# Optimization experiments

Hardware: AMD Instinct MI355X
Metric: run time of the kernel (lower is better)

## Reference

```python
import jax, jax.numpy as jnp
import numpy as np

N = 50000
E = 800000
H = 4
C = 64
EPS = 1e-5

def _gat_layer(x, W, a_src, a_dst, bias, src, dst, n):
    # x: [N, F_in]; W: [F_in, H*C]
    h = (x @ W).reshape(n, H, C)                      # [N,H,C]
    asrc = jnp.einsum('nhc,hc->nh', h, a_src)         # [N,H]
    adst = jnp.einsum('nhc,hc->nh', h, a_dst)         # [N,H]
    e = jax.nn.leaky_relu(asrc[src] + adst[dst], 0.2) # [E,H]
    emax = jax.ops.segment_max(e, dst, num_segments=n)
    e = jnp.exp(e - emax[dst])
    denom = jax.ops.segment_sum(e, dst, num_segments=n)
    alpha = e / (denom[dst] + 1e-16)                  # [E,H]
    msg = h[src] * alpha[:, :, None]                  # [E,H,C]
    out = jax.ops.segment_sum(msg, dst, num_segments=n)
    return out.reshape(n, H * C) + bias

def _bn_eval(x, gamma, beta, mean, var):
    return (x - mean) * jax.lax.rsqrt(var + EPS) * gamma + beta

def setup_inputs() -> dict:
    key = jax.random.key(0)
    ks = jax.random.split(key, 12)
    d = {}
    d['x'] = jax.random.normal(ks[0], (N, 128), jnp.float32)
    d['edge_index'] = jax.random.randint(ks[1], (2, E), 0, N, jnp.int32)
    d['W1'] = jax.random.normal(ks[2], (128, H * C), jnp.float32) * 0.05
    d['a_src1'] = jax.random.normal(ks[3], (H, C), jnp.float32) * 0.05
    d['a_dst1'] = jax.random.normal(ks[4], (H, C), jnp.float32) * 0.05
    d['b1'] = jnp.zeros((H * C,), jnp.float32)
    d['g1'] = jax.random.uniform(ks[5], (H * C,), jnp.float32, 0.5, 1.5)
    d['be1'] = jnp.zeros((H * C,), jnp.float32)
    d['m1'] = jnp.zeros((H * C,), jnp.float32)
    d['v1'] = jax.random.uniform(ks[6], (H * C,), jnp.float32, 0.5, 1.5)
    d['W2'] = jax.random.normal(ks[7], (H * C, H * C), jnp.float32) * 0.05
    d['a_src2'] = jax.random.normal(ks[8], (H, C), jnp.float32) * 0.05
    d['a_dst2'] = jax.random.normal(ks[9], (H, C), jnp.float32) * 0.05
    d['b2'] = jnp.zeros((H * C,), jnp.float32)
    d['g2'] = jax.random.uniform(ks[10], (H * C,), jnp.float32, 0.5, 1.5)
    d['be2'] = jnp.zeros((H * C,), jnp.float32)
    d['m2'] = jnp.zeros((H * C,), jnp.float32)
    d['v2'] = jax.random.uniform(ks[11], (H * C,), jnp.float32, 0.5, 1.5)
    return d

def reference(x, edge_index, W1, a_src1, a_dst1, b1, g1, be1, m1, v1,
              W2, a_src2, a_dst2, b2, g2, be2, m2, v2):
    # PyG GATConv default: add self-loops
    loops = jnp.arange(N, dtype=edge_index.dtype)
    src = jnp.concatenate([edge_index[0], loops])
    dst = jnp.concatenate([edge_index[1], loops])
    h = _gat_layer(x, W1, a_src1, a_dst1, b1, src, dst, N)
    h = jax.nn.relu(_bn_eval(h, g1, be1, m1, v1))  # dropout identity at eval
    h = _gat_layer(h, W2, a_src2, a_dst2, b2, src, dst, N)
    h = jax.nn.relu(_bn_eval(h, g2, be2, m2, v2))
    return jax.nn.log_softmax(h, axis=1)
```

## Files before the change

### kernel.cpp

```cpp
#include <hip/hip_runtime.h>
#include <hip/hip_bf16.h>
#include <cstdint>

#define N_NODES 50000
#define N_EDGES 800000
#define ET_EDGES (N_EDGES + N_NODES)
#define FDIM 256
#define BN_EPS 1e-5f
#define CAP 96

typedef short bf16x8 __attribute__((ext_vector_type(8)));
typedef float f32x4 __attribute__((ext_vector_type(4)));

__device__ __forceinline__ float lrelu(float x) { return x >= 0.f ? x : 0.2f * x; }
__device__ __forceinline__ unsigned short f2b(float f) {
    unsigned int u = __float_as_uint(f);
    u += 0x7fffu + ((u >> 16) & 1u);
    return (unsigned short)(u >> 16);
}

__device__ __forceinline__ void acc_u8(float acc8[8], int2 p, float c) {
    unsigned px = (unsigned)p.x, py = (unsigned)p.y;
#pragma unroll
    for (int k = 0; k < 4; ++k)
        acc8[k] = fmaf((float)((unsigned char)(px >> (8 * k))), c, acc8[k]);
#pragma unroll
    for (int k = 0; k < 4; ++k)
        acc8[k + 4] = fmaf((float)((unsigned char)(py >> (8 * k))), c, acc8[k + 4]);
}

#define PB_Z  196
#define PB_W1 128
#define PB_W2 256
__global__ __launch_bounds__(256) void prep_kernel(
        const float* __restrict__ W1, unsigned short* __restrict__ W1T,
        const float* __restrict__ W2, unsigned short* __restrict__ W2T,
        int* __restrict__ cursor,
        const float* __restrict__ b1, const float* __restrict__ g1,
        const float* __restrict__ be1, const float* __restrict__ m1,
        const float* __restrict__ v1,
        const float* __restrict__ b2, const float* __restrict__ g2,
        const float* __restrict__ be2, const float* __restrict__ m2,
        const float* __restrict__ v2,
        float* sc1, float* sh1, float* sc2, float* sh2) {
    int b = blockIdx.x, tid = threadIdx.x;
    if (b < PB_Z) {
        int i = b * 256 + tid;
        if (i < N_NODES) cursor[i] = 0;
    } else if (b < PB_Z + PB_W1) {
        int t = (b - PB_Z) * 256 + tid;
        int n = t >> 7, k = t & 127;
        W1T[t] = f2b(W1[(size_t)k * 256 + n]);
    } else if (b < PB_Z + PB_W1 + PB_W2) {
        int t = (b - PB_Z - PB_W1) * 256 + tid;
        int n = t >> 8, k = t & 255;
        W2T[t] = f2b(W2[(size_t)k * 256 + n]);
    } else {
        int f = tid;
        float s1 = rsqrtf(v1[f] + BN_EPS) * g1[f];
        sc1[f] = s1;
        sh1[f] = (b1[f] - m1[f]) * s1 + be1[f];
        float s2 = rsqrtf(v2[f] + BN_EPS) * g2[f];
        sc2[f] = s2;
        sh2[f] = (b2[f] - m2[f]) * s2 + be2[f];
    }
}

#define SG_GEMM 782
#define SG_SCAT 3321
#define SG_MIX  (2 * SG_GEMM)
__global__ __launch_bounds__(256) void scat_gemm1_kernel(
        const int* __restrict__ ei, int* __restrict__ cursor, int* __restrict__ csr,
        const float* __restrict__ x,
        const unsigned short* __restrict__ BT,
        const float* __restrict__ a_src, const float* __restrict__ a_dst,
        signed char* __restrict__ H8, float* __restrict__ scaleRow,
        float* __restrict__ asrc, float* __restrict__ adst, int M) {
    constexpr int K = 128;
    constexpr int BK = 64;
    __shared__ unsigned short As[64][BK + 8];
    __shared__ unsigned short Bs[256][BK + 8];
    __shared__ int amaxL[64];
    const int tid = threadIdx.x;
    const int b = blockIdx.x;

    int gemmIdx = -1, scatIdx = 0;
    if (b < SG_MIX) { if (b & 1) gemmIdx = b >> 1; else scatIdx = b >> 1; }
    else scatIdx = b - SG_GEMM;

    if (gemmIdx < 0) {
        int e = scatIdx * 256 + tid;
        if (e < ET_EDGES) {
            int s, d;
            if (e < N_EDGES) { s = ei[e]; d = ei[N_EDGES + e]; }
            else             { s = d = e - N_EDGES; }
            int pos = atomicAdd(&cursor[d], 1);
            if (pos < CAP) csr[d * CAP + pos] = s;
        }
        return;
    }

    const int lane = tid & 63;
    const int w = tid >> 6;
    const int bm = gemmIdx * 64;
    const int wc = w * 64;
    const int hd = w;
    if (tid < 64) amaxL[tid] = 0;

    f32x4 acc[4][4];
#pragma unroll
    for (int i = 0; i < 4; ++i)
#pragma unroll
        for (int j = 0; j < 4; ++j) acc[i][j] = (f32x4){0.f, 0.f, 0.f, 0.f};

    const int srow = tid >> 3;
    const int skc = (tid & 7) * 8;

    for (int k0 = 0; k0 < K; k0 += BK) {
#pragma unroll
        for (int i = 0; i < 2; ++i) {
            int row = i * 32 + srow;
            int ar = bm + row; if (ar >= M) ar = M - 1;
            const float* xp = x + (size_t)ar * K + k0 + skc;
            float4 v0 = *(const float4*)xp;
            float4 v1 = *(const float4*)(xp + 4);
            bf16x8 o;
            o[0] = (short)f2b(v0.x); o[1] = (short)f2b(v0.y);
            o[2] = (short)f2b(v0.z); o[3] = (short)f2b(v0.w);
            o[4] = (short)f2b(v1.x); o[5] = (short)f2b(v1.y);
            o[6] = (short)f2b(v1.z); o[7] = (short)f2b(v1.w);
            *(bf16x8*)&As[row][skc] = o;
        }
#pragma unroll
        for (int i = 0; i < 8; ++i) {
            int row = i * 32 + srow;
            *(bf16x8*)&Bs[row][skc] = *(const bf16x8*)(BT + (size_t)row * K + k0 + skc);
        }
        __syncthreads();
#pragma unroll
        for (int ks = 0; ks < BK; ks += 32) {
            const int kk = ks + (lane >> 4) * 8;
            bf16x8 af[4], bfr[4];
#pragma unroll
            for (int i = 0; i < 4; ++i) {
                af[i]  = *(const bf16x8*)&As[i * 16 + (lane & 15)][kk];
                bfr[i] = *(const bf16x8*)&Bs[wc + i * 16 + (lane & 15)][kk];
            }
#pragma unroll
            for (int i = 0; i < 4; ++i)
#pragma unroll
                for (int j = 0; j < 4; ++j)
                    acc[i][j] = __builtin_amdgcn_mfma_f32_16x16x32_bf16(af[i], bfr[j], acc[i][j], 0, 0, 0);
        }
        __syncthreads();
    }

    const int q = lane >> 4, c16 = lane & 15;
#pragma unroll
    for (int i = 0; i < 4; ++i) {
#pragma unroll
        for (int r = 0; r < 4; ++r) {
            float a = fmaxf(fmaxf(fabsf(acc[i][0][r]), fabsf(acc[i][1][r])),
                            fmaxf(fabsf(acc[i][2][r]), fabsf(acc[i][3][r])));
#pragma unroll
            for (int off = 1; off < 16; off <<= 1) a = fmaxf(a, __shfl_xor(a, off));
            if (c16 == 0) atomicMax(&amaxL[i * 16 + q * 4 + r], __float_as_int(a));
        }
    }
    __syncthreads();

    float asv[4], adv[4];
#pragma unroll
    for (int j = 0; j < 4; ++j) {
        int c = j * 16 + c16;
        asv[j] = a_src[hd * 64 + c];
        adv[j] = a_dst[hd * 64 + c];
    }
#pragma unroll
    for (int i = 0; i < 4; ++i) {
#pragma unroll
        for (int r = 0; r < 4; ++r) {
            int lrow = i * 16 + q * 4 + r;
            int gr = bm + lrow;
            float amax = __int_as_float(amaxL[lrow]);
            float rcpS = amax > 1e-20f ? 127.f / amax : 0.f;
            if (gr < M) {
#pragma unroll
                for (int j = 0; j < 4; ++j) {
                    int qv = (int)rintf(acc[i][j][r] * rcpS);
                    H8[(size_t)gr * 256 + wc + j * 16 + c16] =
                        (signed char)(unsigned char)(qv + 128);
                }
                if (c16 == 0 && w == 0) scaleRow[gr] = amax * (1.f / 127.f);
            }
            float p_s = acc[i][0][r] * asv[0] + acc[i][1][r] * asv[1]
                      + acc[i][2][r] * asv[2] + acc[i][3][r] * asv[3];
            float p_d = acc[i][0][r] * adv[0] + acc[i][1][r] * adv[1]
                      + acc[i][2][r] * adv[2] + acc[i][3][r] * adv[3];
#pragma unroll
            for (int off = 1; off < 16; off <<= 1) {
                p_s += __shfl_xor(p_s, off);
                p_d += __shfl_xor(p_d, off);
            }
            if (c16 == 0 && gr < M) {
                asrc[(size_t)gr * 4 + hd] = p_s;
                adst[(size_t)gr * 4 + hd] = p_d;
            }
        }
    }
}

template <int K>
__global__ __launch_bounds__(256) void gemm_fused_kernel(
        const unsigned short* __restrict__ A,
        const unsigned short* __restrict__ BT,
        const float* __restrict__ a_src, const float* __restrict__ a_dst,
        signed char* __restrict__ H8, float* __restrict__ scaleRow,
        float* __restrict__ asrc, float* __restrict__ adst, int M) {
    constexpr int BK = 64;
    __shared__ unsigned short As[64][BK + 8];
    __shared__ unsigned short Bs[256][BK + 8];
    __shared__ int amaxL[64];
    const int tid = threadIdx.x;
    const int lane = tid & 63;
    const int w = tid >> 6;
    const int bm = blockIdx.x * 64;
    const int wc = w * 64;
    const int hd = w;
    if (tid < 64) amaxL[tid] = 0;

    f32x4 acc[4][4];
#pragma unroll
    for (int i = 0; i < 4; ++i)
#pragma unroll
        for (int j = 0; j < 4; ++j) acc[i][j] = (f32x4){0.f, 0.f, 0.f, 0.f};

    const int srow = tid >> 3;
    const int skc = (tid & 7) * 8;

    for (int k0 = 0; k0 < K; k0 += BK) {
#pragma unroll
        for (int i = 0; i < 2; ++i) {
            int row = i * 32 + srow;
            int ar = bm + row; if (ar >= M) ar = M - 1;
            *(bf16x8*)&As[row][skc] = *(const bf16x8*)(A + (size_t)ar * K + k0 + skc);
        }
#pragma unroll
        for (int i = 0; i < 8; ++i) {
            int row = i * 32 + srow;
            *(bf16x8*)&Bs[row][skc] = *(const bf16x8*)(BT + (size_t)row * K + k0 + skc);
        }
        __syncthreads();
#pragma unroll
        for (int ks = 0; ks < BK; ks += 32) {
            const int kk = ks + (lane >> 4) * 8;
            bf16x8 af[4], bfr[4];
#pragma unroll
            for (int i = 0; i < 4; ++i) {
                af[i]  = *(const bf16x8*)&As[i * 16 + (lane & 15)][kk];
                bfr[i] = *(const bf16x8*)&Bs[wc + i * 16 + (lane & 15)][kk];
            }
#pragma unroll
            for (int i = 0; i < 4; ++i)
#pragma unroll
                for (int j = 0; j < 4; ++j)
                    acc[i][j] = __builtin_amdgcn_mfma_f32_16x16x32_bf16(af[i], bfr[j], acc[i][j], 0, 0, 0);
        }
        __syncthreads();
    }

    const int q = lane >> 4, c16 = lane & 15;
#pragma unroll
    for (int i = 0; i < 4; ++i) {
#pragma unroll
        for (int r = 0; r < 4; ++r) {
            float a = fmaxf(fmaxf(fabsf(acc[i][0][r]), fabsf(acc[i][1][r])),
                            fmaxf(fabsf(acc[i][2][r]), fabsf(acc[i][3][r])));
#pragma unroll
            for (int off = 1; off < 16; off <<= 1) a = fmaxf(a, __shfl_xor(a, off));
            if (c16 == 0) atomicMax(&amaxL[i * 16 + q * 4 + r], __float_as_int(a));
        }
    }
    __syncthreads();

    float asv[4], adv[4];
#pragma unroll
    for (int j = 0; j < 4; ++j) {
        int c = j * 16 + c16;
        asv[j] = a_src[hd * 64 + c];
        adv[j] = a_dst[hd * 64 + c];
    }
#pragma unroll
    for (int i = 0; i < 4; ++i) {
#pragma unroll
        for (int r = 0; r < 4; ++r) {
            int lrow = i * 16 + q * 4 + r;
            int gr = bm + lrow;
            float amax = __int_as_float(amaxL[lrow]);
            float rcpS = amax > 1e-20f ? 127.f / amax : 0.f;
            if (gr < M) {
#pragma unroll
                for (int j = 0; j < 4; ++j) {
                    int qv = (int)rintf(acc[i][j][r] * rcpS);
                    H8[(size_t)gr * 256 + wc + j * 16 + c16] =
                        (signed char)(unsigned char)(qv + 128);
                }
                if (c16 == 0 && w == 0) scaleRow[gr] = amax * (1.f / 127.f);
            }
            float p_s = acc[i][0][r] * asv[0] + acc[i][1][r] * asv[1]
                      + acc[i][2][r] * asv[2] + acc[i][3][r] * asv[3];
            float p_d = acc[i][0][r] * adv[0] + acc[i][1][r] * adv[1]
                      + acc[i][2][r] * adv[2] + acc[i][3][r] * adv[3];
#pragma unroll
            for (int off = 1; off < 16; off <<= 1) {
                p_s += __shfl_xor(p_s, off);
                p_d += __shfl_xor(p_d, off);
            }
            if (c16 == 0 && gr < M) {
                asrc[(size_t)gr * 4 + hd] = p_s;
                adst[(size_t)gr * 4 + hd] = p_d;
            }
        }
    }
}

template <bool FINAL>
__device__ __forceinline__ void gat_epilogue(const float acc8[8], int fl, bool doStore,
                                             int node, const float* __restrict__ scale,
                                             const float* __restrict__ shift,
                                             float* __restrict__ outf,
                                             unsigned short* __restrict__ outb) {
    float4 scA = ((const float4*)scale)[fl * 2], scB = ((const float4*)scale)[fl * 2 + 1];
    float4 shA = ((const float4*)shift)[fl * 2], shB = ((const float4*)shift)[fl * 2 + 1];
    float t[8];
    t[0] = fmaxf(fmaf(acc8[0], scA.x, shA.x), 0.f);
    t[1] = fmaxf(fmaf(acc8[1], scA.y, shA.y), 0.f);
    t[2] = fmaxf(fmaf(acc8[2], scA.z, shA.z), 0.f);
    t[3] = fmaxf(fmaf(acc8[3], scA.w, shA.w), 0.f);
    t[4] = fmaxf(fmaf(acc8[4], scB.x, shB.x), 0.f);
    t[5] = fmaxf(fmaf(acc8[5], scB.y, shB.y), 0.f);
    t[6] = fmaxf(fmaf(acc8[6], scB.z, shB.z), 0.f);
    t[7] = fmaxf(fmaf(acc8[7], scB.w, shB.w), 0.f);
    if (FINAL) {
        float m = t[0];
#pragma unroll
        for (int k = 1; k < 8; ++k) m = fmaxf(m, t[k]);
#pragma unroll
        for (int off = 1; off < 32; off <<= 1) m = fmaxf(m, __shfl_xor(m, off));
        float es = 0.f;
#pragma unroll
        for (int k = 0; k < 8; ++k) es += __expf(t[k] - m);
#pragma unroll
        for (int off = 1; off < 32; off <<= 1) es += __shfl_xor(es, off);
        float lse = m + logf(es);
        if (doStore) {
            float* p = outf + (size_t)node * 256 + fl * 8;
            *(float4*)p = make_float4(t[0] - lse, t[1] - lse, t[2] - lse, t[3] - lse);
            *(float4*)(p + 4) = make_float4(t[4] - lse, t[5] - lse, t[6] - lse, t[7] - lse);
        }
    } else {
        if (doStore) {
            bf16x8 ob;
#pragma unroll
            for (int k = 0; k < 8; ++k) ob[k] = (short)f2b(t[k]);
            *(bf16x8*)(outb + (size_t)node * 256 + fl * 8) = ob;
        }
    }
}

template <bool FINAL>
__global__ __launch_bounds__(256) void gat_gather_kernel(
        const int* __restrict__ cursor,
        const int* __restrict__ csr,
        const float* __restrict__ asrc,
        const float* __restrict__ adst,
        const float* __restrict__ scaleRow,
        const signed char* __restrict__ h8,
        const float* __restrict__ scale,
        const float* __restrict__ shift,
        float* __restrict__ outf,
        unsigned short* __restrict__ outb) {
    __shared__ int2 sa[4][4][65];

    const int wid = threadIdx.x >> 6;
    const int lane = threadIdx.x & 63;
    const int g = lane >> 5, l32 = lane & 31;
    const int hsel = l32 >> 3;
    const unsigned fo = (unsigned)(l32 << 3);

    const int nodeBase = blockIdx.x * 8 + wid * 2;
    if (nodeBase >= N_NODES) return;

    {
        int node = nodeBase + g;
        bool valid = node < N_NODES;
        int nodeC = valid ? node : N_NODES - 1;
        int deg = valid ? min(cursor[nodeC], CAP) : 0;
        int beg = nodeC * CAP;
        int dmax = max(deg, __shfl_xor(deg, 32));

        if (dmax <= 32) {
            float4 ad = *(const float4*)(adst + (size_t)nodeC * 4);
            int s = 0;
            float sc = 0.f;
            float c0 = -3.4e38f, c1 = -3.4e38f, c2 = -3.4e38f, c3 = -3.4e38f;
            if (l32 < deg) {
                s = csr[beg + l32];
                sc = scaleRow[s];
                float4 as = *(const float4*)(asrc + (size_t)s * 4);
                c0 = lrelu(as.x + ad.x); c1 = lrelu(as.y + ad.y);
                c2 = lrelu(as.z + ad.z); c3 = lrelu(as.w + ad.w);
            }
            float m0 = c0, m1 = c1, m2 = c2, m3 = c3;
#pragma unroll
            for (int off = 1; off < 32; off <<= 1) {
                m0 = fmaxf(m0, __shfl_xor(m0, off)); m1 = fmaxf(m1, __shfl_xor(m1, off));
                m2 = fmaxf(m2, __shfl_xor(m2, off)); m3 = fmaxf(m3, __shfl_xor(m3, off));
            }
            float e0 = 0.f, e1 = 0.f, e2 = 0.f, e3 = 0.f;
            if (l32 < deg) {
                e0 = __expf(c0 - m0); e1 = __expf(c1 - m1);
                e2 = __expf(c2 - m2); e3 = __expf(c3 - m3);
            }
            float s0 = e0, s1 = e1, s2 = e2, s3 = e3;
#pragma unroll
            for (int off = 1; off < 32; off <<= 1) {
                s0 += __shfl_xor(s0, off); s1 += __shfl_xor(s1, off);
                s2 += __shfl_xor(s2, off); s3 += __shfl_xor(s3, off);
            }
            float a0 = e0 / (s0 + 1e-16f) * sc, a1 = e1 / (s1 + 1e-16f) * sc;
            float a2 = e2 / (s2 + 1e-16f) * sc, a3 = e3 / (s3 + 1e-16f) * sc;
            sa[wid][0][lane] = make_int2(s, __float_as_int(a0));
            sa[wid][1][lane] = make_int2(s, __float_as_int(a1));
            sa[wid][2][lane] = make_int2(s, __float_as_int(a2));
            sa[wid][3][lane] = make_int2(s, __float_as_int(a3));
            float t0 = a0, t1 = a1, t2 = a2, t3 = a3;
#pragma unroll
            for (int off = 1; off < 32; off <<= 1) {
                t0 += __shfl_xor(t0, off); t1 += __shfl_xor(t1, off);
                t2 += __shfl_xor(t2, off); t3 += __shfl_xor(t3, off);
            }
            float corr = 128.f * (hsel == 0 ? t0 : hsel == 1 ? t1 : hsel == 2 ? t2 : t3);
            __asm__ volatile("s_waitcnt lgkmcnt(0)" ::: "memory");

            const int2* sal = &sa[wid][hsel][g * 32];
            float acc8[8];
#pragma unroll
            for (int k = 0; k < 8; ++k) acc8[k] = 0.f;

            int e = 0;
            for (; e + 7 < deg; e += 8) {
                int2 sv[8]; int2 hv[8];
#pragma unroll
                for (int u = 0; u < 8; ++u) sv[u] = sal[e + u];
#pragma unroll
                for (int u = 0; u < 8; ++u)
                    hv[u] = *(const int2*)(h8 + (((unsigned)sv[u].x << 8) + fo));
#pragma unroll
                for (int u = 0; u < 8; ++u) acc_u8(acc8, hv[u], __int_as_float(sv[u].y));
            }
            for (; e + 3 < deg; e += 4) {
                int2 sv[4]; int2 hv[4];
#pragma unroll
                for (int u = 0; u < 4; ++u) sv[u] = sal[e + u];
#pragma unroll
                for (int u = 0; u < 4; ++u)
                    hv[u] = *(const int2*)(h8 + (((unsigned)sv[u].x << 8) + fo));
#pragma unroll
                for (int u = 0; u < 4; ++u) acc_u8(acc8, hv[u], __int_as_float(sv[u].y));
            }
            for (; e < deg; ++e) {
                int2 sv = sal[e];
                int2 hA = *(const int2*)(h8 + (((unsigned)sv.x << 8) + fo));
                acc_u8(acc8, hA, __int_as_float(sv.y));
            }
#pragma unroll
            for (int k = 0; k < 8; ++k) acc8[k] -= corr;
            gat_epilogue<FINAL>(acc8, l32, valid, node, scale, shift, outf, outb);
            return;
        }
    }

    for (int t = 0; t < 2; ++t) {
        int fnode = nodeBase + t;
        if (fnode >= N_NODES) break;
        int fdeg = min(cursor[fnode], CAP);
        int fbeg = fnode * CAP, fend = fbeg + fdeg;
        float4 ad = *(const float4*)(adst + (size_t)fnode * 4);
        float acc8[8];
#pragma unroll
        for (int k = 0; k < 8; ++k) acc8[k] = 0.f;
        float corr;

        if (fdeg <= 64) {
            int s = 0;
            float sc = 0.f;
            float c0 = -3.4e38f, c1 = -3.4e38f, c2 = -3.4e38f, c3 = -3.4e38f;
            if (lane < fdeg) {
                s = csr[fbeg + lane];
                sc = scaleRow[s];
                float4 as = *(const float4*)(asrc + (size_t)s * 4);
                c0 = lrelu(as.x + ad.x); c1 = lrelu(as.y + ad.y);
                c2 = lrelu(as.z + ad.z); c3 = lrelu(as.w + ad.w);
            }
            float m0 = c0, m1 = c1, m2 = c2, m3 = c3;
#pragma unroll
            for (int off = 1; off < 64; off <<= 1) {
                m0 = fmaxf(m0, __shfl_xor(m0, off)); m1 = fmaxf(m1, __shfl_xor(m1, off));
                m2 = fmaxf(m2, __shfl_xor(m2, off)); m3 = fmaxf(m3, __shfl_xor(m3, off));
            }
            float e0 = 0.f, e1 = 0.f, e2 = 0.f, e3 = 0.f;
            if (lane < fdeg) {
                e0 = __expf(c0 - m0); e1 = __expf(c1 - m1);
                e2 = __expf(c2 - m2); e3 = __expf(c3 - m3);
            }
            float s0 = e0, s1 = e1, s2 = e2, s3 = e3;
#pragma unroll
            for (int off = 1; off < 64; off <<= 1) {
                s0 += __shfl_xor(s0, off); s1 += __shfl_xor(s1, off);
                s2 += __shfl_xor(s2, off); s3 += __shfl_xor(s3, off);
            }
            float a0 = e0 / (s0 + 1e-16f) * sc, a1 = e1 / (s1 + 1e-16f) * sc;
            float a2 = e2 / (s2 + 1e-16f) * sc, a3 = e3 / (s3 + 1e-16f) * sc;
            sa[wid][0][lane] = make_int2(s, __float_as_int(a0));
            sa[wid][1][lane] = make_int2(s, __float_as_int(a1));
            sa[wid][2][lane] = make_int2(s, __float_as_int(a2));
            sa[wid][3][lane] = make_int2(s, __float_as_int(a3));
            float t0 = a0, t1 = a1, t2 = a2, t3 = a3;
#pragma unroll
            for (int off = 1; off < 64; off <<= 1) {
                t0 += __shfl_xor(t0, off); t1 += __shfl_xor(t1, off);
                t2 += __shfl_xor(t2, off); t3 += __shfl_xor(t3, off);
            }
            corr = 128.f * (hsel == 0 ? t0 : hsel == 1 ? t1 : hsel == 2 ? t2 : t3);
            __asm__ volatile("s_waitcnt lgkmcnt(0)" ::: "memory");

            const int2* sal = &sa[wid][hsel][0];
            int e = 0;
            for (; e + 1 < fdeg; e += 2) {
                int2 sv = sal[e + g];
                int2 hA = *(const int2*)(h8 + (((unsigned)sv.x << 8) + fo));
                acc_u8(acc8, hA, __int_as_float(sv.y));
            }
            if (e < fdeg) {
                int idx = e + g;
                int2 sv = sal[idx < fdeg ? idx : 0];
                float aA = idx < fdeg ? __int_as_float(sv.y) : 0.f;
                int2 hA = *(const int2*)(h8 + (((unsigned)sv.x << 8) + fo));
                acc_u8(acc8, hA, aA);
            }
#pragma unroll
            for (int k = 0; k < 8; ++k) acc8[k] += __shfl_xor(acc8[k], 32);
        } else {
            float m0 = -3.4e38f, m1 = -3.4e38f, m2 = -3.4e38f, m3 = -3.4e38f;
            for (int e = fbeg + lane; e < fend; e += 64) {
                int s = csr[e];
                float4 as = *(const float4*)(asrc + (size_t)s * 4);
                m0 = fmaxf(m0, lrelu(as.x + ad.x)); m1 = fmaxf(m1, lrelu(as.y + ad.y));
                m2 = fmaxf(m2, lrelu(as.z + ad.z)); m3 = fmaxf(m3, lrelu(as.w + ad.w));
            }
#pragma unroll
            for (int off = 1; off < 64; off <<= 1) {
                m0 = fmaxf(m0, __shfl_xor(m0, off)); m1 = fmaxf(m1, __shfl_xor(m1, off));
                m2 = fmaxf(m2, __shfl_xor(m2, off)); m3 = fmaxf(m3, __shfl_xor(m3, off));
            }
            float s0 = 0.f, s1 = 0.f, s2 = 0.f, s3 = 0.f;
            for (int e = fbeg + lane; e < fend; e += 64) {
                int s = csr[e];
                float4 as = *(const float4*)(asrc + (size_t)s * 4);
                s0 += __expf(lrelu(as.x + ad.x) - m0); s1 += __expf(lrelu(as.y + ad.y) - m1);
                s2 += __expf(lrelu(as.z + ad.z) - m2); s3 += __expf(lrelu(as.w + ad.w) - m3);
            }
#pragma unroll
            for (int off = 1; off < 64; off <<= 1) {
                s0 += __shfl_xor(s0, off); s1 += __shfl_xor(s1, off);
                s2 += __shfl_xor(s2, off); s3 += __shfl_xor(s3, off);
            }
            float mh = (hsel == 0) ? m0 : (hsel == 1) ? m1 : (hsel == 2) ? m2 : m3;
            float rh = (hsel == 0) ? 1.f / (s0 + 1e-16f) : (hsel == 1) ? 1.f / (s1 + 1e-16f)
                     : (hsel == 2) ? 1.f / (s2 + 1e-16f) : 1.f / (s3 + 1e-16f);
            float adh = (hsel == 0) ? ad.x : (hsel == 1) ? ad.y : (hsel == 2) ? ad.z : ad.w;
            float asumL = 0.f;
            for (int e = fbeg; e < fend; ++e) {
                int s = csr[e];
                float ash = asrc[(size_t)s * 4 + hsel];
                float a = __expf(lrelu(ash + adh) - mh) * rh * scaleRow[s];
                asumL += a;
                int2 hv = *(const int2*)(h8 + (((unsigned)s << 8) + fo));
                acc_u8(acc8, hv, a);
            }
            corr = 128.f * asumL;
        }
#pragma unroll
        for (int k = 0; k < 8; ++k) acc8[k] -= corr;
        gat_epilogue<FINAL>(acc8, l32, g == 0, fnode, scale, shift, outf, outb);
    }
}

extern "C" void kernel_launch(void* const* d_in, const int* in_sizes, int n_in,
                              void* d_out, int out_size, void* d_ws, size_t ws_size,
                              hipStream_t stream) {
    (void)in_sizes; (void)n_in; (void)out_size; (void)ws_size;
    const float* x   = (const float*)d_in[0];
    const int*   ei  = (const int*)d_in[1];
    const float* W1  = (const float*)d_in[2];
    const float* as1 = (const float*)d_in[3];
    const float* ad1 = (const float*)d_in[4];
    const float* b1  = (const float*)d_in[5];
    const float* g1  = (const float*)d_in[6];
    const float* be1 = (const float*)d_in[7];
    const float* m1  = (const float*)d_in[8];
    const float* v1  = (const float*)d_in[9];
    const float* W2  = (const float*)d_in[10];
    const float* as2 = (const float*)d_in[11];
    const float* ad2 = (const float*)d_in[12];
    const float* b2  = (const float*)d_in[13];
    const float* g2  = (const float*)d_in[14];
    const float* be2 = (const float*)d_in[15];
    const float* m2  = (const float*)d_in[16];
    const float* v2  = (const float*)d_in[17];

    float* out = (float*)d_out;
    unsigned short* actb = (unsigned short*)d_out;

    char* base = (char*)d_ws;
    signed char* h8 = (signed char*)base;          base += (size_t)N_NODES * 256;
    float* scaleRow = (float*)base;                base += (size_t)N_NODES * 4;
    base += (size_t)N_NODES * 128 * 2;
    float* asrc = (float*)base;                    base += (size_t)N_NODES * 4 * 4;
    float* adst = (float*)base;                    base += (size_t)N_NODES * 4 * 4;
    float* sc1 = (float*)base;                     base += 1024;
    float* sh1 = (float*)base;                     base += 1024;
    float* sc2 = (float*)base;                     base += 1024;
    float* sh2 = (float*)base;                     base += 1024;
    unsigned short* W1T = (unsigned short*)base;   base += 256 * 128 * 2;
    unsigned short* W2T = (unsigned short*)base;   base += 256 * 256 * 2;
    int* cursor = (int*)base;                      base += N_NODES * 4;
    int* csr  = (int*)base;

    prep_kernel<<<PB_Z + PB_W1 + PB_W2 + 1, 256, 0, stream>>>(
        W1, W1T, W2, W2T, cursor,
        b1, g1, be1, m1, v1, b2, g2, be2, m2, v2, sc1, sh1, sc2, sh2);

    const int nb = (N_NODES + 7) / 8;
    const int gb = (N_NODES + 63) / 64;

    scat_gemm1_kernel<<<SG_SCAT + SG_GEMM, 256, 0, stream>>>(
        ei, cursor, csr, x, W1T, as1, ad1, h8, scaleRow, asrc, adst, N_NODES);

    gat_gather_kernel<false><<<nb, 256, 0, stream>>>(cursor, csr, asrc, adst, scaleRow, h8,
                                                     sc1, sh1, nullptr, actb);

    gemm_fused_kernel<256><<<gb, 256, 0, stream>>>(actb, W2T, as2, ad2, h8, scaleRow,
                                                   asrc, adst, N_NODES);

    gat_gather_kernel<true><<<nb, 256, 0, stream>>>(cursor, csr, asrc, adst, scaleRow, h8,
                                                    sc2, sh2, out, nullptr);
}
```

Baseline: 291.1 us.

## Process four nodes per wave and prefetch both pairs' edge metadata up front

Each wave now handles two node pairs instead of one, halving the grid. The csr index, scaleRow, asrc and adst loads for both pairs are issued before any softmax work, so the dependent gather latency of the second pair overlaps with the first. The csr loads are now unconditional with clamped source indices, which touches padding slots. The cost is more registers, fewer waves in flight, and the second pair reusing the same LDS slot.

```diff
diff --git a/kernel.cpp b/kernel.cpp
--- a/kernel.cpp
+++ b/kernel.cpp
@@ -369,6 +369,214 @@
 }
 
 template <bool FINAL>
+__device__ __forceinline__ void gat_pair_fast(
+        int pairBase, int g, int l32, int hsel, unsigned fo,
+        bool valid, int deg, unsigned s, float sc, float4 as, float4 ad,
+        int2 (*saw)[65],
+        const signed char* __restrict__ h8,
+        const float* __restrict__ scale, const float* __restrict__ shift,
+        float* __restrict__ outf, unsigned short* __restrict__ outb) {
+    const int lane = g * 32 + l32;
+    int node = pairBase + g;
+    float c0 = -3.4e38f, c1 = -3.4e38f, c2 = -3.4e38f, c3 = -3.4e38f;
+    if (l32 < deg) {
+        c0 = lrelu(as.x + ad.x); c1 = lrelu(as.y + ad.y);
+        c2 = lrelu(as.z + ad.z); c3 = lrelu(as.w + ad.w);
+    }
+    float m0 = c0, m1 = c1, m2 = c2, m3 = c3;
+#pragma unroll
+    for (int off = 1; off < 32; off <<= 1) {
+        m0 = fmaxf(m0, __shfl_xor(m0, off)); m1 = fmaxf(m1, __shfl_xor(m1, off));
+        m2 = fmaxf(m2, __shfl_xor(m2, off)); m3 = fmaxf(m3, __shfl_xor(m3, off));
+    }
+    float e0 = 0.f, e1 = 0.f, e2 = 0.f, e3 = 0.f;
+    if (l32 < deg) {
+        e0 = __expf(c0 - m0); e1 = __expf(c1 - m1);
+        e2 = __expf(c2 - m2); e3 = __expf(c3 - m3);
+    }
+    float s0 = e0, s1 = e1, s2 = e2, s3 = e3;
+#pragma unroll
+    for (int off = 1; off < 32; off <<= 1) {
+        s0 += __shfl_xor(s0, off); s1 += __shfl_xor(s1, off);
+        s2 += __shfl_xor(s2, off); s3 += __shfl_xor(s3, off);
+    }
+    float a0 = e0 / (s0 + 1e-16f) * sc, a1 = e1 / (s1 + 1e-16f) * sc;
+    float a2 = e2 / (s2 + 1e-16f) * sc, a3 = e3 / (s3 + 1e-16f) * sc;
+    saw[0][lane] = make_int2((int)s, __float_as_int(a0));
+    saw[1][lane] = make_int2((int)s, __float_as_int(a1));
+    saw[2][lane] = make_int2((int)s, __float_as_int(a2));
+    saw[3][lane] = make_int2((int)s, __float_as_int(a3));
+    float t0 = a0, t1 = a1, t2 = a2, t3 = a3;
+#pragma unroll
+    for (int off = 1; off < 32; off <<= 1) {
+        t0 += __shfl_xor(t0, off); t1 += __shfl_xor(t1, off);
+        t2 += __shfl_xor(t2, off); t3 += __shfl_xor(t3, off);
+    }
+    float corr = 128.f * (hsel == 0 ? t0 : hsel == 1 ? t1 : hsel == 2 ? t2 : t3);
+    __asm__ volatile("s_waitcnt lgkmcnt(0)" ::: "memory");
+
+    const int2* sal = &saw[hsel][g * 32];
+    float acc8[8];
+#pragma unroll
+    for (int k = 0; k < 8; ++k) acc8[k] = 0.f;
+
+    int e = 0;
+    for (; e + 7 < deg; e += 8) {
+        int2 sv[8]; int2 hv[8];
+#pragma unroll
+        for (int u = 0; u < 8; ++u) sv[u] = sal[e + u];
+#pragma unroll
+        for (int u = 0; u < 8; ++u)
+            hv[u] = *(const int2*)(h8 + (((unsigned)sv[u].x << 8) + fo));
+#pragma unroll
+        for (int u = 0; u < 8; ++u) acc_u8(acc8, hv[u], __int_as_float(sv[u].y));
+    }
+    for (; e + 3 < deg; e += 4) {
+        int2 sv[4]; int2 hv[4];
+#pragma unroll
+        for (int u = 0; u < 4; ++u) sv[u] = sal[e + u];
+#pragma unroll
+        for (int u = 0; u < 4; ++u)
+            hv[u] = *(const int2*)(h8 + (((unsigned)sv[u].x << 8) + fo));
+#pragma unroll
+        for (int u = 0; u < 4; ++u) acc_u8(acc8, hv[u], __int_as_float(sv[u].y));
+    }
+    for (; e < deg; ++e) {
+        int2 sv = sal[e];
+        int2 hA = *(const int2*)(h8 + (((unsigned)sv.x << 8) + fo));
+        acc_u8(acc8, hA, __int_as_float(sv.y));
+    }
+#pragma unroll
+    for (int k = 0; k < 8; ++k) acc8[k] -= corr;
+    gat_epilogue<FINAL>(acc8, l32, valid, node, scale, shift, outf, outb);
+}
+
+template <bool FINAL>
+__device__ __forceinline__ void gat_pair_fallback(
+        int pairBase, int lane, int g, int l32, int hsel, unsigned fo,
+        int2 (*saw)[65],
+        const int* __restrict__ cursor, const int* __restrict__ csr,
+        const float* __restrict__ asrc, const float* __restrict__ adst,
+        const float* __restrict__ scaleRow, const signed char* __restrict__ h8,
+        const float* __restrict__ scale, const float* __restrict__ shift,
+        float* __restrict__ outf, unsigned short* __restrict__ outb) {
+    for (int t = 0; t < 2; ++t) {
+        int fnode = pairBase + t;
+        if (fnode >= N_NODES) break;
+        int fdeg = min(cursor[fnode], CAP);
+        int fbeg = fnode * CAP, fend = fbeg + fdeg;
+        float4 ad = *(const float4*)(adst + (size_t)fnode * 4);
+        float acc8[8];
+#pragma unroll
+        for (int k = 0; k < 8; ++k) acc8[k] = 0.f;
+        float corr;
+
+        if (fdeg <= 64) {
+            int s = 0;
+            float sc = 0.f;
+            float c0 = -3.4e38f, c1 = -3.4e38f, c2 = -3.4e38f, c3 = -3.4e38f;
+            if (lane < fdeg) {
+                s = csr[fbeg + lane];
+                sc = scaleRow[s];
+                float4 as = *(const float4*)(asrc + (size_t)s * 4);
+                c0 = lrelu(as.x + ad.x); c1 = lrelu(as.y + ad.y);
+                c2 = lrelu(as.z + ad.z); c3 = lrelu(as.w + ad.w);
+            }
+            float m0 = c0, m1 = c1, m2 = c2, m3 = c3;
+#pragma unroll
+            for (int off = 1; off < 64; off <<= 1) {
+                m0 = fmaxf(m0, __shfl_xor(m0, off)); m1 = fmaxf(m1, __shfl_xor(m1, off));
+                m2 = fmaxf(m2, __shfl_xor(m2, off)); m3 = fmaxf(m3, __shfl_xor(m3, off));
+            }
+            float e0 = 0.f, e1 = 0.f, e2 = 0.f, e3 = 0.f;
+            if (lane < fdeg) {
+                e0 = __expf(c0 - m0); e1 = __expf(c1 - m1);
+                e2 = __expf(c2 - m2); e3 = __expf(c3 - m3);
+            }
+            float s0 = e0, s1 = e1, s2 = e2, s3 = e3;
+#pragma unroll
+            for (int off = 1; off < 64; off <<= 1) {
+                s0 += __shfl_xor(s0, off); s1 += __shfl_xor(s1, off);
+                s2 += __shfl_xor(s2, off); s3 += __shfl_xor(s3, off);
+            }
+            float a0 = e0 / (s0 + 1e-16f) * sc, a1 = e1 / (s1 + 1e-16f) * sc;
+            float a2 = e2 / (s2 + 1e-16f) * sc, a3 = e3 / (s3 + 1e-16f) * sc;
+            saw[0][lane] = make_int2(s, __float_as_int(a0));
+            saw[1][lane] = make_int2(s, __float_as_int(a1));
+            saw[2][lane] = make_int2(s, __float_as_int(a2));
+            saw[3][lane] = make_int2(s, __float_as_int(a3));
+            float t0 = a0, t1 = a1, t2 = a2, t3 = a3;
+#pragma unroll
+            for (int off = 1; off < 64; off <<= 1) {
+                t0 += __shfl_xor(t0, off); t1 += __shfl_xor(t1, off);
+                t2 += __shfl_xor(t2, off); t3 += __shfl_xor(t3, off);
+            }
+            corr = 128.f * (hsel == 0 ? t0 : hsel == 1 ? t1 : hsel == 2 ? t2 : t3);
+            __asm__ volatile("s_waitcnt lgkmcnt(0)" ::: "memory");
+
+            const int2* sal = &saw[hsel][0];
+            int e = 0;
+            for (; e + 1 < fdeg; e += 2) {
+                int2 sv = sal[e + g];
+                int2 hA = *(const int2*)(h8 + (((unsigned)sv.x << 8) + fo));
+                acc_u8(acc8, hA, __int_as_float(sv.y));
+            }
+            if (e < fdeg) {
+                int idx = e + g;
+                int2 sv = sal[idx < fdeg ? idx : 0];
+                float aA = idx < fdeg ? __int_as_float(sv.y) : 0.f;
+                int2 hA = *(const int2*)(h8 + (((unsigned)sv.x << 8) + fo));
+                acc_u8(acc8, hA, aA);
+            }
+#pragma unroll
+            for (int k = 0; k < 8; ++k) acc8[k] += __shfl_xor(acc8[k], 32);
+        } else {
+            float m0 = -3.4e38f, m1 = -3.4e38f, m2 = -3.4e38f, m3 = -3.4e38f;
+            for (int e = fbeg + lane; e < fend; e += 64) {
+                int s = csr[e];
+                float4 as = *(const float4*)(asrc + (size_t)s * 4);
+                m0 = fmaxf(m0, lrelu(as.x + ad.x)); m1 = fmaxf(m1, lrelu(as.y + ad.y));
+                m2 = fmaxf(m2, lrelu(as.z + ad.z)); m3 = fmaxf(m3, lrelu(as.w + ad.w));
+            }
+#pragma unroll
+            for (int off = 1; off < 64; off <<= 1) {
+                m0 = fmaxf(m0, __shfl_xor(m0, off)); m1 = fmaxf(m1, __shfl_xor(m1, off));
+                m2 = fmaxf(m2, __shfl_xor(m2, off)); m3 = fmaxf(m3, __shfl_xor(m3, off));
+            }
+            float s0 = 0.f, s1 = 0.f, s2 = 0.f, s3 = 0.f;
+            for (int e = fbeg + lane; e < fend; e += 64) {
+                int s = csr[e];
+                float4 as = *(const float4*)(asrc + (size_t)s * 4);
+                s0 += __expf(lrelu(as.x + ad.x) - m0); s1 += __expf(lrelu(as.y + ad.y) - m1);
+                s2 += __expf(lrelu(as.z + ad.z) - m2); s3 += __expf(lrelu(as.w + ad.w) - m3);
+            }
+#pragma unroll
+            for (int off = 1; off < 64; off <<= 1) {
+                s0 += __shfl_xor(s0, off); s1 += __shfl_xor(s1, off);
+                s2 += __shfl_xor(s2, off); s3 += __shfl_xor(s3, off);
+            }
+            float mh = (hsel == 0) ? m0 : (hsel == 1) ? m1 : (hsel == 2) ? m2 : m3;
+            float rh = (hsel == 0) ? 1.f / (s0 + 1e-16f) : (hsel == 1) ? 1.f / (s1 + 1e-16f)
+                     : (hsel == 2) ? 1.f / (s2 + 1e-16f) : 1.f / (s3 + 1e-16f);
+            float adh = (hsel == 0) ? ad.x : (hsel == 1) ? ad.y : (hsel == 2) ? ad.z : ad.w;
+            float asumL = 0.f;
+            for (int e = fbeg; e < fend; ++e) {
+                int s = csr[e];
+                float ash = asrc[(size_t)s * 4 + hsel];
+                float a = __expf(lrelu(ash + adh) - mh) * rh * scaleRow[s];
+                asumL += a;
+                int2 hv = *(const int2*)(h8 + (((unsigned)s << 8) + fo));
+                acc_u8(acc8, hv, a);
+            }
+            corr = 128.f * asumL;
+        }
+#pragma unroll
+        for (int k = 0; k < 8; ++k) acc8[k] -= corr;
+        gat_epilogue<FINAL>(acc8, l32, g == 0, fnode, scale, shift, outf, outb);
+    }
+}
+
+template <bool FINAL>
 __global__ __launch_bounds__(256) void gat_gather_kernel(
         const int* __restrict__ cursor,
         const int* __restrict__ csr,
@@ -388,213 +596,40 @@
     const int hsel = l32 >> 3;
     const unsigned fo = (unsigned)(l32 << 3);
 
-    const int nodeBase = blockIdx.x * 8 + wid * 2;
-    if (nodeBase >= N_NODES) return;
-
-    {
-        int node = nodeBase + g;
-        bool valid = node < N_NODES;
-        int nodeC = valid ? node : N_NODES - 1;
-        int deg = valid ? min(cursor[nodeC], CAP) : 0;
-        int beg = nodeC * CAP;
-        int dmax = max(deg, __shfl_xor(deg, 32));
-
-        if (dmax <= 32) {
-            float4 ad = *(const float4*)(adst + (size_t)nodeC * 4);
-            int s = 0;
-            float sc = 0.f;
-            float c0 = -3.4e38f, c1 = -3.4e38f, c2 = -3.4e38f, c3 = -3.4e38f;
-            if (l32 < deg) {
-                s = csr[beg + l32];
-                sc = scaleRow[s];
-                float4 as = *(const float4*)(asrc + (size_t)s * 4);
-                c0 = lrelu(as.x + ad.x); c1 = lrelu(as.y + ad.y);
-                c2 = lrelu(as.z + ad.z); c3 = lrelu(as.w + ad.w);
-            }
-            float m0 = c0, m1 = c1, m2 = c2, m3 = c3;
-#pragma unroll
-            for (int off = 1; off < 32; off <<= 1) {
-                m0 = fmaxf(m0, __shfl_xor(m0, off)); m1 = fmaxf(m1, __shfl_xor(m1, off));
-                m2 = fmaxf(m2, __shfl_xor(m2, off)); m3 = fmaxf(m3, __shfl_xor(m3, off));
-            }
-            float e0 = 0.f, e1 = 0.f, e2 = 0.f, e3 = 0.f;
-            if (l32 < deg) {
-                e0 = __expf(c0 - m0); e1 = __expf(c1 - m1);
-                e2 = __expf(c2 - m2); e3 = __expf(c3 - m3);
-            }
-            float s0 = e0, s1 = e1, s2 = e2, s3 = e3;
-#pragma unroll
-            for (int off = 1; off < 32; off <<= 1) {
-                s0 += __shfl_xor(s0, off); s1 += __shfl_xor(s1, off);
-                s2 += __shfl_xor(s2, off); s3 += __shfl_xor(s3, off);
-            }
-            float a0 = e0 / (s0 + 1e-16f) * sc, a1 = e1 / (s1 + 1e-16f) * sc;
-            float a2 = e2 / (s2 + 1e-16f) * sc, a3 = e3 / (s3 + 1e-16f) * sc;
-            sa[wid][0][lane] = make_int2(s, __float_as_int(a0));
-            sa[wid][1][lane] = make_int2(s, __float_as_int(a1));
-            sa[wid][2][lane] = make_int2(s, __float_as_int(a2));
-            sa[wid][3][lane] = make_int2(s, __float_as_int(a3));
-            float t0 = a0, t1 = a1, t2 = a2, t3 = a3;
-#pragma unroll
-            for (int off = 1; off < 32; off <<= 1) {
-                t0 += __shfl_xor(t0, off); t1 += __shfl_xor(t1, off);
-                t2 += __shfl_xor(t2, off); t3 += __shfl_xor(t3, off);
-            }
-            float corr = 128.f * (hsel == 0 ? t0 : hsel == 1 ? t1 : hsel == 2 ? t2 : t3);
-            __asm__ volatile("s_waitcnt lgkmcnt(0)" ::: "memory");
-
-            const int2* sal = &sa[wid][hsel][g * 32];
-            float acc8[8];
-#pragma unroll
-            for (int k = 0; k < 8; ++k) acc8[k] = 0.f;
-
-            int e = 0;
-            for (; e + 7 < deg; e += 8) {
-                int2 sv[8]; int2 hv[8];
-#pragma unroll
-                for (int u = 0; u < 8; ++u) sv[u] = sal[e + u];
-#pragma unroll
-                for (int u = 0; u < 8; ++u)
-                    hv[u] = *(const int2*)(h8 + (((unsigned)sv[u].x << 8) + fo));
-#pragma unroll
-                for (int u = 0; u < 8; ++u) acc_u8(acc8, hv[u], __int_as_float(sv[u].y));
-            }
-            for (; e + 3 < deg; e += 4) {
-                int2 sv[4]; int2 hv[4];
-#pragma unroll
-                for (int u = 0; u < 4; ++u) sv[u] = sal[e + u];
-#pragma unroll
-                for (int u = 0; u < 4; ++u)
-                    hv[u] = *(const int2*)(h8 + (((unsigned)sv[u].x << 8) + fo));
-#pragma unroll
-                for (int u = 0; u < 4; ++u) acc_u8(acc8, hv[u], __int_as_float(sv[u].y));
-            }
-            for (; e < deg; ++e) {
-                int2 sv = sal[e];
-                int2 hA = *(const int2*)(h8 + (((unsigned)sv.x << 8) + fo));
-                acc_u8(acc8, hA, __int_as_float(sv.y));
-            }
-#pragma unroll
-            for (int k = 0; k < 8; ++k) acc8[k] -= corr;
-            gat_epilogue<FINAL>(acc8, l32, valid, node, scale, shift, outf, outb);
-            return;
-        }
-    }
-
-    for (int t = 0; t < 2; ++t) {
-        int fnode = nodeBase + t;
-        if (fnode >= N_NODES) break;
-        int fdeg = min(cursor[fnode], CAP);
-        int fbeg = fnode * CAP, fend = fbeg + fdeg;
-        float4 ad = *(const float4*)(adst + (size_t)fnode * 4);
-        float acc8[8];
-#pragma unroll
-        for (int k = 0; k < 8; ++k) acc8[k] = 0.f;
-        float corr;
-
-        if (fdeg <= 64) {
-            int s = 0;
-            float sc = 0.f;
-            float c0 = -3.4e38f, c1 = -3.4e38f, c2 = -3.4e38f, c3 = -3.4e38f;
-            if (lane < fdeg) {
-                s = csr[fbeg + lane];
-                sc = scaleRow[s];
-                float4 as = *(const float4*)(asrc + (size_t)s * 4);
-                c0 = lrelu(as.x + ad.x); c1 = lrelu(as.y + ad.y);
-                c2 = lrelu(as.z + ad.z); c3 = lrelu(as.w + ad.w);
-            }
-            float m0 = c0, m1 = c1, m2 = c2, m3 = c3;
-#pragma unroll
-            for (int off = 1; off < 64; off <<= 1) {
-                m0 = fmaxf(m0, __shfl_xor(m0, off)); m1 = fmaxf(m1, __shfl_xor(m1, off));
-                m2 = fmaxf(m2, __shfl_xor(m2, off)); m3 = fmaxf(m3, __shfl_xor(m3, off));
-            }
-            float e0 = 0.f, e1 = 0.f, e2 = 0.f, e3 = 0.f;
-            if (lane < fdeg) {
-                e0 = __expf(c0 - m0); e1 = __expf(c1 - m1);
-                e2 = __expf(c2 - m2); e3 = __expf(c3 - m3);
-            }
-            float s0 = e0, s1 = e1, s2 = e2, s3 = e3;
-#pragma unroll
-            for (int off = 1; off < 64; off <<= 1) {
-                s0 += __shfl_xor(s0, off); s1 += __shfl_xor(s1, off);
-                s2 += __shfl_xor(s2, off); s3 += __shfl_xor(s3, off);
-            }
-            float a0 = e0 / (s0 + 1e-16f) * sc, a1 = e1 / (s1 + 1e-16f) * sc;
-            float a2 = e2 / (s2 + 1e-16f) * sc, a3 = e3 / (s3 + 1e-16f) * sc;
-            sa[wid][0][lane] = make_int2(s, __float_as_int(a0));
-            sa[wid][1][lane] = make_int2(s, __float_as_int(a1));
-            sa[wid][2][lane] = make_int2(s, __float_as_int(a2));
-            sa[wid][3][lane] = make_int2(s, __float_as_int(a3));
-            float t0 = a0, t1 = a1, t2 = a2, t3 = a3;
-#pragma unroll
-            for (int off = 1; off < 64; off <<= 1) {
-                t0 += __shfl_xor(t0, off); t1 += __shfl_xor(t1, off);
-                t2 += __shfl_xor(t2, off); t3 += __shfl_xor(t3, off);
-            }
-            corr = 128.f * (hsel == 0 ? t0 : hsel == 1 ? t1 : hsel == 2 ? t2 : t3);
-            __asm__ volatile("s_waitcnt lgkmcnt(0)" ::: "memory");
-
-            const int2* sal = &sa[wid][hsel][0];
-            int e = 0;
-            for (; e + 1 < fdeg; e += 2) {
-                int2 sv = sal[e + g];
-                int2 hA = *(const int2*)(h8 + (((unsigned)sv.x << 8) + fo));
-                acc_u8(acc8, hA, __int_as_float(sv.y));
-            }
-            if (e < fdeg) {
-                int idx = e + g;
-                int2 sv = sal[idx < fdeg ? idx : 0];
-                float aA = idx < fdeg ? __int_as_float(sv.y) : 0.f;
-                int2 hA = *(const int2*)(h8 + (((unsigned)sv.x << 8) + fo));
-                acc_u8(acc8, hA, aA);
-            }
-#pragma unroll
-            for (int k = 0; k < 8; ++k) acc8[k] += __shfl_xor(acc8[k], 32);
-        } else {
-            float m0 = -3.4e38f, m1 = -3.4e38f, m2 = -3.4e38f, m3 = -3.4e38f;
-            for (int e = fbeg + lane; e < fend; e += 64) {
-                int s = csr[e];
-                float4 as = *(const float4*)(asrc + (size_t)s * 4);
-                m0 = fmaxf(m0, lrelu(as.x + ad.x)); m1 = fmaxf(m1, lrelu(as.y + ad.y));
-                m2 = fmaxf(m2, lrelu(as.z + ad.z)); m3 = fmaxf(m3, lrelu(as.w + ad.w));
-            }
-#pragma unroll
-            for (int off = 1; off < 64; off <<= 1) {
-                m0 = fmaxf(m0, __shfl_xor(m0, off)); m1 = fmaxf(m1, __shfl_xor(m1, off));
-                m2 = fmaxf(m2, __shfl_xor(m2, off)); m3 = fmaxf(m3, __shfl_xor(m3, off));
-            }
-            float s0 = 0.f, s1 = 0.f, s2 = 0.f, s3 = 0.f;
-            for (int e = fbeg + lane; e < fend; e += 64) {
-                int s = csr[e];
-                float4 as = *(const float4*)(asrc + (size_t)s * 4);
-                s0 += __expf(lrelu(as.x + ad.x) - m0); s1 += __expf(lrelu(as.y + ad.y) - m1);
-                s2 += __expf(lrelu(as.z + ad.z) - m2); s3 += __expf(lrelu(as.w + ad.w) - m3);
-            }
-#pragma unroll
-            for (int off = 1; off < 64; off <<= 1) {
-                s0 += __shfl_xor(s0, off); s1 += __shfl_xor(s1, off);
-                s2 += __shfl_xor(s2, off); s3 += __shfl_xor(s3, off);
-            }
-            float mh = (hsel == 0) ? m0 : (hsel == 1) ? m1 : (hsel == 2) ? m2 : m3;
-            float rh = (hsel == 0) ? 1.f / (s0 + 1e-16f) : (hsel == 1) ? 1.f / (s1 + 1e-16f)
-                     : (hsel == 2) ? 1.f / (s2 + 1e-16f) : 1.f / (s3 + 1e-16f);
-            float adh = (hsel == 0) ? ad.x : (hsel == 1) ? ad.y : (hsel == 2) ? ad.z : ad.w;
-            float asumL = 0.f;
-            for (int e = fbeg; e < fend; ++e) {
-                int s = csr[e];
-                float ash = asrc[(size_t)s * 4 + hsel];
-                float a = __expf(lrelu(ash + adh) - mh) * rh * scaleRow[s];
-                asumL += a;
-                int2 hv = *(const int2*)(h8 + (((unsigned)s << 8) + fo));
-                acc_u8(acc8, hv, a);
-            }
-            corr = 128.f * asumL;
-        }
-#pragma unroll
-        for (int k = 0; k < 8; ++k) acc8[k] -= corr;
-        gat_epilogue<FINAL>(acc8, l32, g == 0, fnode, scale, shift, outf, outb);
-    }
+    const int quadBase = blockIdx.x * 16 + wid * 4;
+    if (quadBase >= N_NODES) return;
+
+    int nA = quadBase + g,      nB = quadBase + 2 + g;
+    bool vA = nA < N_NODES,     vB = nB < N_NODES;
+    int cA = vA ? nA : N_NODES - 1, cB = vB ? nB : N_NODES - 1;
+    int degA = vA ? min(cursor[cA], CAP) : 0;
+    int degB = vB ? min(cursor[cB], CAP) : 0;
+    unsigned sA = min((unsigned)csr[cA * CAP + l32], (unsigned)(N_NODES - 1));
+    unsigned sB = min((unsigned)csr[cB * CAP + l32], (unsigned)(N_NODES - 1));
+    float scA = scaleRow[sA],   scB = scaleRow[sB];
+    float4 asA = *(const float4*)(asrc + (size_t)sA * 4);
+    float4 asB = *(const float4*)(asrc + (size_t)sB * 4);
+    float4 adA = *(const float4*)(adst + (size_t)cA * 4);
+    float4 adB = *(const float4*)(adst + (size_t)cB * 4);
+    int dmaxA = max(degA, __shfl_xor(degA, 32));
+    int dmaxB = max(degB, __shfl_xor(degB, 32));
+
+    if (dmaxA <= 32)
+        gat_pair_fast<FINAL>(quadBase, g, l32, hsel, fo, vA, degA, sA, scA, asA, adA,
+                             sa[wid], h8, scale, shift, outf, outb);
+    else
+        gat_pair_fallback<FINAL>(quadBase, lane, g, l32, hsel, fo, sa[wid],
+                                 cursor, csr, asrc, adst, scaleRow, h8,
+                                 scale, shift, outf, outb);
+
+    if (quadBase + 2 >= N_NODES) return;
+    if (dmaxB <= 32)
+        gat_pair_fast<FINAL>(quadBase + 2, g, l32, hsel, fo, vB, degB, sB, scB, asB, adB,
+                             sa[wid], h8, scale, shift, outf, outb);
+    else
+        gat_pair_fallback<FINAL>(quadBase + 2, lane, g, l32, hsel, fo, sa[wid],
+                                 cursor, csr, asrc, adst, scaleRow, h8,
+                                 scale, shift, outf, outb);
 }
 
 extern "C" void kernel_launch(void* const* d_in, const int* in_sizes, int n_in,
@@ -642,7 +677,7 @@
         W1, W1T, W2, W2T, cursor,
         b1, g1, be1, m1, v1, b2, g2, be2, m2, v2, sc1, sh1, sc2, sh2);
 
-    const int nb = (N_NODES + 7) / 8;
+    const int nb = (N_NODES + 15) / 16;
     const int gb = (N_NODES + 63) / 64;
 
     scat_gemm1_kernel<<<SG_SCAT + SG_GEMM, 256, 0, stream>>>(
```

After: 300.4 us. 1.03x slower.
